# Performance work log

Measured on AMD Instinct MI355X. Metric: run time of the kernel, lower is better.

Reference implementation:

```python
import jax, jax.numpy as jnp
import numpy as np

D = 1024      # model dim
H = 16        # num heads
HD = D // H   # head dim = 64
B, N, M = 4, 4096, 256
EPS = 1e-12   # torch F.normalize eps


def setup_inputs() -> dict:
    key = jax.random.key(0)
    ks = jax.random.split(key, 11)
    s = 0.02  # weight init scale
    W = lambda k: jax.random.normal(k, (D, D), jnp.float32) * s
    return {
        "x": jax.random.normal(ks[0], (B, N, D), jnp.float32),
        "c": jax.random.normal(ks[1], (B, M, D), jnp.float32),
        "Wq_x": W(ks[2]), "Wk_x": W(ks[3]), "Wv_x": W(ks[4]),
        "Wq_c": W(ks[5]), "Wk_c": W(ks[6]), "Wv_c": W(ks[7]),
        "Wo_x": W(ks[8]), "Wo_c": W(ks[9]),
        "norm_const": 0.5 * jnp.ones((1, H, 1, 1), jnp.float32),
    }


def _heads(t):
    # (B, S, D) -> (B, H, S, HD)
    b, s, _ = t.shape
    return t.reshape(b, s, H, HD).transpose(0, 2, 1, 3)


def _l2norm(t):
    n = jnp.linalg.norm(t, axis=-1, keepdims=True)
    return t / jnp.maximum(n, EPS)


def reference(x, c, Wq_x, Wk_x, Wv_x, Wq_c, Wk_c, Wv_c, Wo_x, Wo_c, norm_const):
    b, n, d = x.shape
    m = c.shape[1]
    # fused QKV projections for each stream (Linear, no bias: y = t @ W^T)
    qx = _l2norm(_heads(x @ Wq_x.T))   # (B,H,N,HD), cosine-normalized
    kx = _l2norm(_heads(x @ Wk_x.T))
    vx = _heads(x @ Wv_x.T)
    qc = _l2norm(_heads(c @ Wq_c.T))   # (B,H,M,HD)
    kc = _l2norm(_heads(c @ Wk_c.T))
    vc = _heads(c @ Wv_c.T)
    # concat streams along the sequence axis
    q = jnp.concatenate([qx, qc], axis=2)   # (B,H,N+M,HD)
    k = jnp.concatenate([kx, kc], axis=2)
    v = jnp.concatenate([vx, vc], axis=2)
    n_tot = n + m
    # cosine (linear) attention, non-causal: values scaled by N^sigmoid(norm_const)
    v = v / (jnp.float32(n_tot) ** jax.nn.sigmoid(norm_const))
    kv = jnp.einsum("bhnd,bhne->bhde", k, v)         # (B,H,HD,HD)
    attn = jnp.einsum("bhnd,bhde->bhne", q, kv)      # (B,H,N+M,HD)
    # split streams, merge heads, output projections
    attn_x = attn[:, :, :n].transpose(0, 2, 1, 3).reshape(b, n, H * HD)
    attn_c = attn[:, :, n:].transpose(0, 2, 1, 3).reshape(b, m, H * HD)
    out_x = attn_x @ Wo_x.T
    out_c = attn_c @ Wo_c.T
    return out_x, out_c
```

## Files before the change

kernel.cpp:

```cpp
#include <hip/hip_runtime.h>
#include <cstdint>

typedef unsigned int u32;
typedef unsigned short u16;
typedef float fx4 __attribute__((ext_vector_type(4)));
typedef __bf16 bfx8 __attribute__((ext_vector_type(8)));

__device__ __forceinline__ u16 f2bf(float f) {
  u32 u = __builtin_bit_cast(u32, f);
  u32 r = (u + 0x7fffu + ((u >> 16) & 1u)) >> 16;
  return (u16)r;
}
__device__ __forceinline__ float bf2f(u16 v) {
  return __builtin_bit_cast(float, (u32)v << 16);
}
__device__ __forceinline__ void async_copy16(const void* g, void* l) {
  auto gp = reinterpret_cast<__attribute__((address_space(1))) void*>((uintptr_t)g);
  auto lp = reinterpret_cast<__attribute__((address_space(3))) void*>((uintptr_t)l);
  __builtin_amdgcn_global_load_lds(gp, lp, 16, 0, 0);
}

__global__ __launch_bounds__(256) void cvt_all(
    const float* __restrict__ x, const float* __restrict__ c,
    const float* __restrict__ w0, const float* __restrict__ w1,
    const float* __restrict__ w2, const float* __restrict__ w3,
    const float* __restrict__ w4, const float* __restrict__ w5,
    const float* __restrict__ w6, const float* __restrict__ w7,
    u16* __restrict__ xb, u16* __restrict__ cb, u16* __restrict__ wb) {
  const int i = blockIdx.x * 256 + threadIdx.x;
  const float* src;
  u16* dst;
  size_t off;
  if (i < 4194304) {
    src = x; dst = xb; off = (size_t)i;
  } else if (i < 4456448) {
    src = c; dst = cb; off = (size_t)(i - 4194304);
  } else {
    const int r = i - 4456448;
    const int wsel = r >> 18;
    off = (size_t)(r & 262143);
    switch (wsel) {
      case 0: src = w0; break; case 1: src = w1; break;
      case 2: src = w2; break; case 3: src = w3; break;
      case 4: src = w4; break; case 5: src = w5; break;
      case 6: src = w6; break; default: src = w7; break;
    }
    dst = wb + (size_t)wsel * 1048576;
  }
  const fx4 v = *(const fx4*)(src + off * 4);
  uint2 o;
  o.x = (u32)f2bf(v[0]) | ((u32)f2bf(v[1]) << 16);
  o.y = (u32)f2bf(v[2]) | ((u32)f2bf(v[3]) << 16);
  *(uint2*)(dst + off * 4) = o;
}

__device__ __forceinline__ void gemm256_core(
    const u16* __restrict__ A, const u16* __restrict__ Bw,
    long rowBase, long colBase, u16* lds, fx4 (&acc)[8][4]) {
  const int t = threadIdx.x;
  const int lane = t & 63;
  const int lr = lane & 15;
  const int quad = lane >> 4;
  const int w = t >> 6;
  const int wr = w >> 2;
  const int wc = w & 3;

  const int fA0 = t * 8;
  int dA[2];
  const u16* gA[2];
  const u16* gB[2];
#pragma unroll
  for (int r = 0; r < 2; ++r) {
    const int f = fA0 + r * 4096;
    const int row = f >> 5;
    const int gst = (f >> 3) & 3;
    const int scol = ((gst ^ (row & 3)) << 3);
    dA[r] = f;
    gA[r] = A + (size_t)(rowBase + row) * 1024 + scol;
    gB[r] = Bw + (size_t)(colBase + row) * 1024 + scol;
  }
  const int swk = (quad ^ (lr & 3)) << 3;
  const int abase = (wr * 128 + lr) * 32 + swk;
  const int bbase = 8192 + (wc * 64 + lr) * 32 + swk;

#pragma unroll
  for (int pt = 0; pt < 3; ++pt) {
    u16* slot = lds + pt * 16384;
#pragma unroll
    for (int r = 0; r < 2; ++r) {
      async_copy16(gA[r] + pt * 32, slot + dA[r]);
      async_copy16(gB[r] + pt * 32, slot + 8192 + dA[r]);
    }
  }
  asm volatile("s_waitcnt vmcnt(8)" ::: "memory");
  __builtin_amdgcn_s_barrier();
  __builtin_amdgcn_sched_barrier(0);

  for (int tt = 0; tt < 32; ++tt) {
    u16* slot = lds + (tt & 3) * 16384;
    bfx8 bfr[4], af[4];
#pragma unroll
    for (int i = 0; i < 4; ++i) bfr[i] = *(const bfx8*)(slot + bbase + i * 512);
#pragma unroll
    for (int i = 0; i < 4; ++i) af[i] = *(const bfx8*)(slot + abase + i * 512);
    if (tt < 29) {
      u16* nslot = lds + ((tt + 3) & 3) * 16384;
      const int ko = (tt + 3) * 32;
#pragma unroll
      for (int r = 0; r < 2; ++r) {
        async_copy16(gA[r] + ko, nslot + dA[r]);
        async_copy16(gB[r] + ko, nslot + 8192 + dA[r]);
      }
    }
    __builtin_amdgcn_s_setprio(1);
#pragma unroll
    for (int mi = 0; mi < 4; ++mi)
#pragma unroll
      for (int ni = 0; ni < 4; ++ni)
        acc[mi][ni] =
            __builtin_amdgcn_mfma_f32_16x16x32_bf16(af[mi], bfr[ni], acc[mi][ni], 0, 0, 0);
    __builtin_amdgcn_s_setprio(0);
#pragma unroll
    for (int i = 0; i < 4; ++i)
      af[i] = *(const bfx8*)(slot + abase + 2048 + i * 512);
    __builtin_amdgcn_s_setprio(1);
#pragma unroll
    for (int mi = 0; mi < 4; ++mi)
#pragma unroll
      for (int ni = 0; ni < 4; ++ni)
        acc[4 + mi][ni] =
            __builtin_amdgcn_mfma_f32_16x16x32_bf16(af[mi], bfr[ni], acc[4 + mi][ni], 0, 0, 0);
    __builtin_amdgcn_s_setprio(0);
    __builtin_amdgcn_sched_barrier(0);
    if (tt < 29) {
      asm volatile("s_waitcnt vmcnt(8) lgkmcnt(0)" ::: "memory");
      __builtin_amdgcn_s_barrier();
    } else if (tt == 29) {
      asm volatile("s_waitcnt vmcnt(4) lgkmcnt(0)" ::: "memory");
      __builtin_amdgcn_s_barrier();
    } else if (tt == 30) {
      asm volatile("s_waitcnt vmcnt(0) lgkmcnt(0)" ::: "memory");
      __builtin_amdgcn_s_barrier();
    }
    __builtin_amdgcn_sched_barrier(0);
  }
}

__global__ __launch_bounds__(512, 2) void proj_fused(
    const u16* __restrict__ Xb, const u16* __restrict__ Cb, const u16* __restrict__ Wb,
    u16* __restrict__ Qx, u16* __restrict__ Qc,
    u16* __restrict__ Kt, u16* __restrict__ Vt,
    const float* __restrict__ nc) {
  extern __shared__ __align__(16) u16 lds[];
  const bool isC = blockIdx.y >= 64;
  const u16* A = isC ? Cb : Xb;
  const u16* Bw = Wb + (isC ? 3145728 : 0);
  const long rowBase = (long)(isC ? blockIdx.y - 64 : blockIdx.y) * 256;
  const long colBase = (long)blockIdx.x * 256;

  fx4 acc[8][4] = {};
  gemm256_core(A, Bw, rowBase, colBase, lds, acc);

  const int t = threadIdx.x;
  const int lane = t & 63;
  const int lr = lane & 15;
  const int quad = lane >> 4;
  const int w = t >> 6;
  const int wr = w >> 2;
  const int wc = w & 3;
  const long wRowBase = rowBase + wr * 128;

  const long col0 = colBase + wc * 64;
  const int col64 = (int)(col0 >> 6);
  const int sel = col64 >> 4;
  const int h = col64 & 15;
  const int lcolBase = (int)(col0 & 1023);

  if (sel == 0) {
    u16* dst = isC ? Qc : Qx;
#pragma unroll
    for (int mi = 0; mi < 8; ++mi) {
      float ss[4] = {0.f, 0.f, 0.f, 0.f};
#pragma unroll
      for (int ni = 0; ni < 4; ++ni)
#pragma unroll
        for (int r = 0; r < 4; ++r) ss[r] += acc[mi][ni][r] * acc[mi][ni][r];
#pragma unroll
      for (int off = 1; off < 16; off <<= 1)
#pragma unroll
        for (int r = 0; r < 4; ++r) ss[r] += __shfl_xor(ss[r], off, 64);
      float sc[4];
#pragma unroll
      for (int r = 0; r < 4; ++r) sc[r] = 1.f / fmaxf(sqrtf(ss[r]), 1e-12f);
#pragma unroll
      for (int ni = 0; ni < 4; ++ni) {
        const long col = lcolBase + ni * 16 + lr;
#pragma unroll
        for (int r = 0; r < 4; ++r) {
          const long row = wRowBase + mi * 16 + quad * 4 + r;
          dst[row * 1024 + col] = f2bf(acc[mi][ni][r] * sc[r]);
        }
      }
    }
  } else {
    __syncthreads();
    u16* LT = lds + w * 8192;
    u16* T = (sel == 1) ? Kt : Vt;
    int b, nglob0;
    if (!isC) { b = (int)(wRowBase >> 12); nglob0 = (int)(wRowBase & 4095); }
    else      { b = (int)(wRowBase >> 8);  nglob0 = 4096 + (int)(wRowBase & 255); }
    u16* Tw = T + (size_t)(b * 16 + h) * 64 * 4352;
    const float vs = __expf(-8.3783908f / (1.f + __expf(-nc[h])));

#pragma unroll
    for (int mi = 0; mi < 8; ++mi) {
      float sc[4];
      if (sel == 1) {
        float ss[4] = {0.f, 0.f, 0.f, 0.f};
#pragma unroll
        for (int ni = 0; ni < 4; ++ni)
#pragma unroll
          for (int r = 0; r < 4; ++r) ss[r] += acc[mi][ni][r] * acc[mi][ni][r];
#pragma unroll
        for (int off = 1; off < 16; off <<= 1)
#pragma unroll
          for (int r = 0; r < 4; ++r) ss[r] += __shfl_xor(ss[r], off, 64);
#pragma unroll
        for (int r = 0; r < 4; ++r) sc[r] = 1.f / fmaxf(sqrtf(ss[r]), 1e-12f);
      } else {
#pragma unroll
        for (int r = 0; r < 4; ++r) sc[r] = vs;
      }
      const int g = mi * 2 + (quad >> 1);
      const int sub = (quad & 1) * 4;
#pragma unroll
      for (int ni = 0; ni < 4; ++ni) {
        const int d = ni * 16 + lr;
        uint2 o;
        o.x = (u32)f2bf(acc[mi][ni][0] * sc[0]) | ((u32)f2bf(acc[mi][ni][1] * sc[1]) << 16);
        o.y = (u32)f2bf(acc[mi][ni][2] * sc[2]) | ((u32)f2bf(acc[mi][ni][3] * sc[3]) << 16);
        *(uint2*)&LT[d * 128 + ((g ^ (d & 15)) << 3) + sub] = o;
      }
    }
    __syncthreads();
    const int d = lane;
    u16* drow = Tw + (size_t)d * 4352 + nglob0;
#pragma unroll
    for (int j = 0; j < 16; ++j) {
      const uint4 qv = *(const uint4*)&LT[d * 128 + ((j ^ (d & 15)) << 3)];
      *(uint4*)&drow[j * 8] = qv;
    }
  }
}

__global__ __launch_bounds__(256) void kv_mfma(
    const u16* __restrict__ Kt, const u16* __restrict__ Vt, float* __restrict__ kvb) {
  __shared__ __align__(16) u16 TT[4][2][4096];
  const int bh = blockIdx.x;
  const int t = threadIdx.x;
  const int w = t >> 6;
  const int lane = t & 63;
  const int lr = lane & 15;
  const int quad = lane >> 4;
  const u16* Ksrc = Kt + (size_t)bh * 64 * 4352;
  const u16* Vsrc = Vt + (size_t)bh * 64 * 4352;
  const int row8 = lane >> 3;
  const int gst = lane & 7;
  fx4 acc[4][4] = {};

  for (int s = 0; s < 17; ++s) {
    const int kbase = w * 1088 + s * 64;
#pragma unroll
    for (int i = 0; i < 8; ++i) {
      const int row = i * 8 + row8;
      const int col = ((gst ^ (row & 7)) << 3);
      const size_t go = (size_t)row * 4352 + kbase + col;
      async_copy16(Ksrc + go, &TT[w][0][i * 512 + lane * 8]);
      async_copy16(Vsrc + go, &TT[w][1][i * 512 + lane * 8]);
    }
    __syncthreads();
#pragma unroll
    for (int ks = 0; ks < 2; ++ks) {
      bfx8 af[4], bfr[4];
      const int g = ((ks * 4 + quad) ^ (lr & 7)) << 3;
#pragma unroll
      for (int i = 0; i < 4; ++i) af[i] = *(const bfx8*)&TT[w][0][(i * 16 + lr) * 64 + g];
#pragma unroll
      for (int i = 0; i < 4; ++i) bfr[i] = *(const bfx8*)&TT[w][1][(i * 16 + lr) * 64 + g];
#pragma unroll
      for (int mi = 0; mi < 4; ++mi)
#pragma unroll
        for (int ni = 0; ni < 4; ++ni)
          acc[mi][ni] =
              __builtin_amdgcn_mfma_f32_16x16x32_bf16(af[mi], bfr[ni], acc[mi][ni], 0, 0, 0);
    }
    __syncthreads();
  }
  float* red = (float*)&TT[0][0][0];
  float* my = red + w * 4096;
#pragma unroll
  for (int mi = 0; mi < 4; ++mi)
#pragma unroll
    for (int ni = 0; ni < 4; ++ni) {
      const int e = ni * 16 + lr;
      const int dg = mi * 4 + quad;
      *(fx4*)&my[e * 64 + ((dg ^ (e & 15)) << 2)] = acc[mi][ni];
    }
  __syncthreads();
  float* outp = kvb + (size_t)bh * 4096;
#pragma unroll
  for (int j = 0; j < 4; ++j) {
    const int L = t * 16 + j * 4;
    const int e = L >> 6;
    const int dg = (L >> 2) & 15;
    const int addr = e * 64 + ((dg ^ (e & 15)) << 2);
    fx4 sv = *(const fx4*)&red[addr];
    sv += *(const fx4*)&red[4096 + addr];
    sv += *(const fx4*)&red[8192 + addr];
    sv += *(const fx4*)&red[12288 + addr];
    *(fx4*)&outp[L] = sv;
  }
}

__global__ __launch_bounds__(256) void weff_build(
    const u16* __restrict__ WoX, const u16* __restrict__ WoC,
    const float* __restrict__ kvb, u16* __restrict__ WeffX, u16* __restrict__ WeffC) {
  const int ot = blockIdx.x;
  const int bh = blockIdx.y;
  const int b = bh >> 4, h = bh & 15;
  const u16* Wo = blockIdx.z ? WoC : WoX;
  u16* outp = (blockIdx.z ? WeffC : WeffX) + (size_t)b * 1048576;

  __shared__ __align__(16) float kvT[64 * 64];
  __shared__ __align__(16) float WoT[64 * 64];
  const int t = threadIdx.x;
#pragma unroll
  for (int j = 0; j < 4; ++j) {
    const int idx = (t + 256 * j) * 4;
    *(fx4*)&kvT[idx] = *(const fx4*)&kvb[(size_t)bh * 4096 + idx];
  }
#pragma unroll
  for (int j = 0; j < 2; ++j) {
    const int u = t + 256 * j;
    const int row = u >> 3;
    const int e0 = (u & 7) * 8;
    const uint4 q = *(const uint4*)&Wo[(size_t)(ot * 64 + row) * 1024 + h * 64 + e0];
    WoT[(e0 + 0) * 64 + row] = bf2f((u16)(q.x & 0xffff));
    WoT[(e0 + 1) * 64 + row] = bf2f((u16)(q.x >> 16));
    WoT[(e0 + 2) * 64 + row] = bf2f((u16)(q.y & 0xffff));
    WoT[(e0 + 3) * 64 + row] = bf2f((u16)(q.y >> 16));
    WoT[(e0 + 4) * 64 + row] = bf2f((u16)(q.z & 0xffff));
    WoT[(e0 + 5) * 64 + row] = bf2f((u16)(q.z >> 16));
    WoT[(e0 + 6) * 64 + row] = bf2f((u16)(q.w & 0xffff));
    WoT[(e0 + 7) * 64 + row] = bf2f((u16)(q.w >> 16));
  }
  __syncthreads();
  const int ob = (t >> 4) * 4;
  const int db = (t & 15) * 4;
  float acc[4][4] = {};
#pragma unroll 4
  for (int e = 0; e < 64; ++e) {
    const fx4 wv = *(const fx4*)&WoT[e * 64 + ob];
    const fx4 kvv = *(const fx4*)&kvT[e * 64 + db];
#pragma unroll
    for (int i = 0; i < 4; ++i)
#pragma unroll
      for (int j = 0; j < 4; ++j)
        acc[i][j] += wv[i] * kvv[j];
  }
#pragma unroll
  for (int i = 0; i < 4; ++i)
#pragma unroll
    for (int j = 0; j < 4; ++j)
      outp[(size_t)(ot * 64 + ob + i) * 1024 + h * 64 + db + j] = f2bf(acc[i][j]);
}

__global__ __launch_bounds__(512, 2) void out_fused(
    const u16* __restrict__ Qx, const u16* __restrict__ Qc,
    const u16* __restrict__ Wex, const u16* __restrict__ Wec,
    float* __restrict__ out) {
  extern __shared__ __align__(16) u16 lds[];
  const int yt = blockIdx.y;
  const int b = yt / 17;
  const int l = yt - b * 17;
  const bool isC = (l == 16);
  const u16* A;
  const u16* Bw;
  float* C;
  long rowBase;
  if (!isC) {
    A = Qx + (size_t)b * 4194304;
    Bw = Wex + (size_t)b * 1048576;
    C = out + (size_t)b * 4194304;
    rowBase = (long)l * 256;
  } else {
    A = Qc + (size_t)b * 262144;
    Bw = Wec + (size_t)b * 1048576;
    C = out + 16777216 + (size_t)b * 262144;
    rowBase = 0;
  }
  const long colBase = (long)blockIdx.x * 256;

  fx4 acc[8][4] = {};
  gemm256_core(A, Bw, rowBase, colBase, lds, acc);

  const int t = threadIdx.x;
  const int lane = t & 63;
  const int lr = lane & 15;
  const int quad = lane >> 4;
  const int w = t >> 6;
  const int wr = w >> 2;
  const int wc = w & 3;
#pragma unroll
  for (int mi = 0; mi < 8; ++mi)
#pragma unroll
    for (int ni = 0; ni < 4; ++ni) {
      const long col = colBase + wc * 64 + ni * 16 + lr;
#pragma unroll
      for (int r = 0; r < 4; ++r) {
        const long row = rowBase + wr * 128 + mi * 16 + quad * 4 + r;
        C[row * 1024 + col] = acc[mi][ni][r];
      }
    }
}

extern "C" void kernel_launch(void* const* d_in, const int* in_sizes, int n_in,
                              void* d_out, int out_size, void* d_ws, size_t ws_size,
                              hipStream_t stream) {
  (void)in_sizes; (void)n_in; (void)out_size; (void)ws_size;
  const float* x = (const float*)d_in[0];
  const float* c = (const float*)d_in[1];
  const float* nc = (const float*)d_in[10];
  float* out = (float*)d_out;
  char* ws = (char*)d_ws;

  static bool attr_done = false;
  if (!attr_done) {
    hipFuncSetAttribute((const void*)proj_fused,
                        hipFuncAttributeMaxDynamicSharedMemorySize, 131072);
    hipFuncSetAttribute((const void*)out_fused,
                        hipFuncAttributeMaxDynamicSharedMemorySize, 131072);
    attr_done = true;
  }

  u16* Xb = (u16*)(ws + 0);
  u16* Cb = (u16*)(ws + 33554432);
  u16* Wb = (u16*)(ws + 35651584);
  u16* Qx = (u16*)(ws + 52428800);
  u16* Qc = (u16*)(ws + 85983232);
  u16* Kt = (u16*)(ws + 88080384);
  u16* Vt = (u16*)(ws + 123731968);
  float* kvb = (float*)(ws + 159383552);
  u16* Weffx = (u16*)(ws + 160432128);
  u16* Weffc = (u16*)(ws + 168820736);

  cvt_all<<<25600, 256, 0, stream>>>(
      x, c, (const float*)d_in[2], (const float*)d_in[3], (const float*)d_in[4],
      (const float*)d_in[5], (const float*)d_in[6], (const float*)d_in[7],
      (const float*)d_in[8], (const float*)d_in[9], Xb, Cb, Wb);

  proj_fused<<<dim3(12, 68), 512, 131072, stream>>>(Xb, Cb, Wb, Qx, Qc, Kt, Vt, nc);
  kv_mfma<<<64, 256, 0, stream>>>(Kt, Vt, kvb);
  weff_build<<<dim3(16, 64, 2), 256, 0, stream>>>(Wb + 6 * 1048576, Wb + 7 * 1048576,
                                                  kvb, Weffx, Weffc);
  out_fused<<<dim3(4, 68), 512, 131072, stream>>>(Qx, Qc, Weffx, Weffc, out);
}
```

Before: 419.3 us.

## Restructure GEMM mainloop into 8-phase ping-pong schedule with new LDS swizzle

Rewrites the 256x256 bf16 GEMM core so that each iteration covers two 64-wide K blocks split into eight phases. Each phase interleaves LDS reads, async global-to-LDS copies of half an operand tile, and one half of the MFMA work, with a barrier between every phase. The LDS layout also changes: two rows are packed per 64-element line, with an XOR swizzle meant to reduce bank conflicts. The goal is finer overlap of global loads with MFMA and fewer LDS stalls, at the cost of more barriers and more complex wait-count bookkeeping, which risks errors.

```diff
diff --git a/kernel.cpp b/kernel.cpp
--- a/kernel.cpp
+++ b/kernel.cpp
@@ -54,8 +54,35 @@
   *(uint2*)(dst + off * 4) = o;
 }
 
+#define GC_DSB(BUF, KS)                                                        \
+  _Pragma("unroll") for (int i_ = 0; i_ < 4; ++i_) bfr[i_] =                   \
+      *(const bfx8*)(lds + (BUF) + 16384 + (KS) * 8192 + wc * 2048 + i_ * 512 + aLane);
+#define GC_DSA(BUF, KS, H)                                                     \
+  _Pragma("unroll") for (int i_ = 0; i_ < 4; ++i_) af[i_] =                    \
+      *(const bfx8*)(lds + (BUF) + (KS) * 8192 + wr * 4096 + (H) * 2048 + i_ * 512 + aLane);
+#define GC_STA(REG, KCOL)                                                      \
+  async_copy16(Aop + aOff0 + (KCOL), lds + (REG) + dst0);                      \
+  async_copy16(Aop + aOff1 + (KCOL), lds + (REG) + dst1);
+#define GC_STB(REG, KCOL)                                                      \
+  async_copy16(Bop + bOff0 + (KCOL), lds + (REG) + dst0);                      \
+  async_copy16(Bop + bOff1 + (KCOL), lds + (REG) + dst1);
+#define GC_MFMA(H)                                                             \
+  __builtin_amdgcn_s_setprio(1);                                               \
+  _Pragma("unroll") for (int mi_ = 0; mi_ < 4; ++mi_)                          \
+  _Pragma("unroll") for (int ni_ = 0; ni_ < 4; ++ni_)                          \
+      acc[(H) * 4 + mi_][ni_] = __builtin_amdgcn_mfma_f32_16x16x32_bf16(       \
+          af[mi_], bfr[ni_], acc[(H) * 4 + mi_][ni_], 0, 0, 0);                \
+  __builtin_amdgcn_s_setprio(0);
+#define GC_MID()                                                               \
+  __builtin_amdgcn_s_barrier();                                                \
+  asm volatile("s_waitcnt lgkmcnt(0)" ::: "memory");                           \
+  __builtin_amdgcn_sched_barrier(0);
+#define GC_END()                                                               \
+  __builtin_amdgcn_s_barrier();                                                \
+  __builtin_amdgcn_sched_barrier(0);
+
 __device__ __forceinline__ void gemm256_core(
-    const u16* __restrict__ A, const u16* __restrict__ Bw,
+    const u16* __restrict__ Aop, const u16* __restrict__ Bop,
     long rowBase, long colBase, u16* lds, fx4 (&acc)[8][4]) {
   const int t = threadIdx.x;
   const int lane = t & 63;
@@ -64,85 +91,84 @@
   const int w = t >> 6;
   const int wr = w >> 2;
   const int wc = w & 3;
-
-  const int fA0 = t * 8;
-  int dA[2];
-  const u16* gA[2];
-  const u16* gB[2];
-#pragma unroll
-  for (int r = 0; r < 2; ++r) {
-    const int f = fA0 + r * 4096;
-    const int row = f >> 5;
-    const int gst = (f >> 3) & 3;
-    const int scol = ((gst ^ (row & 3)) << 3);
-    dA[r] = f;
-    gA[r] = A + (size_t)(rowBase + row) * 1024 + scol;
-    gB[r] = Bw + (size_t)(colBase + row) * 1024 + scol;
-  }
-  const int swk = (quad ^ (lr & 3)) << 3;
-  const int abase = (wr * 128 + lr) * 32 + swk;
-  const int bbase = 8192 + (wc * 64 + lr) * 32 + swk;
-
-#pragma unroll
-  for (int pt = 0; pt < 3; ++pt) {
-    u16* slot = lds + pt * 16384;
-#pragma unroll
-    for (int r = 0; r < 2; ++r) {
-      async_copy16(gA[r] + pt * 32, slot + dA[r]);
-      async_copy16(gB[r] + pt * 32, slot + 8192 + dA[r]);
-    }
-  }
+  const int phys = (((lr & 1) << 2) | quad) ^ ((lr >> 1) & 7);
+  const int aLane = ((lr >> 1) << 6) + (phys << 3);
+
+  int aOff0, aOff1, bOff0, bOff1, dst0, dst1;
+  {
+    const int c0 = t;
+    const int R0 = c0 >> 3;
+    const int lg0 = (c0 & 7) ^ (R0 & 7);
+    const int m0_ = 2 * R0 + (lg0 >> 2);
+    const int g0 = lg0 & 3;
+    aOff0 = (int)(rowBase + m0_) * 1024 + g0 * 8;
+    bOff0 = (int)(colBase + m0_) * 1024 + g0 * 8;
+    dst0 = c0 * 8;
+    const int c1 = t + 512;
+    const int R1 = c1 >> 3;
+    const int lg1 = (c1 & 7) ^ (R1 & 7);
+    const int m1_ = 2 * R1 + (lg1 >> 2);
+    const int g1 = lg1 & 3;
+    aOff1 = (int)(rowBase + m1_) * 1024 + g1 * 8;
+    bOff1 = (int)(colBase + m1_) * 1024 + g1 * 8;
+    dst1 = c1 * 8;
+  }
+
+  GC_STA(0, 0) GC_STB(16384, 0) GC_STA(8192, 32) GC_STB(24576, 32)
+  GC_STA(32768, 64) GC_STB(49152, 64)
   asm volatile("s_waitcnt vmcnt(8)" ::: "memory");
   __builtin_amdgcn_s_barrier();
   __builtin_amdgcn_sched_barrier(0);
 
-  for (int tt = 0; tt < 32; ++tt) {
-    u16* slot = lds + (tt & 3) * 16384;
-    bfx8 bfr[4], af[4];
-#pragma unroll
-    for (int i = 0; i < 4; ++i) bfr[i] = *(const bfx8*)(slot + bbase + i * 512);
-#pragma unroll
-    for (int i = 0; i < 4; ++i) af[i] = *(const bfx8*)(slot + abase + i * 512);
-    if (tt < 29) {
-      u16* nslot = lds + ((tt + 3) & 3) * 16384;
-      const int ko = (tt + 3) * 32;
-#pragma unroll
-      for (int r = 0; r < 2; ++r) {
-        async_copy16(gA[r] + ko, nslot + dA[r]);
-        async_copy16(gB[r] + ko, nslot + 8192 + dA[r]);
-      }
-    }
-    __builtin_amdgcn_s_setprio(1);
-#pragma unroll
-    for (int mi = 0; mi < 4; ++mi)
-#pragma unroll
-      for (int ni = 0; ni < 4; ++ni)
-        acc[mi][ni] =
-            __builtin_amdgcn_mfma_f32_16x16x32_bf16(af[mi], bfr[ni], acc[mi][ni], 0, 0, 0);
-    __builtin_amdgcn_s_setprio(0);
-#pragma unroll
-    for (int i = 0; i < 4; ++i)
-      af[i] = *(const bfx8*)(slot + abase + 2048 + i * 512);
-    __builtin_amdgcn_s_setprio(1);
-#pragma unroll
-    for (int mi = 0; mi < 4; ++mi)
-#pragma unroll
-      for (int ni = 0; ni < 4; ++ni)
-        acc[4 + mi][ni] =
-            __builtin_amdgcn_mfma_f32_16x16x32_bf16(af[mi], bfr[ni], acc[4 + mi][ni], 0, 0, 0);
-    __builtin_amdgcn_s_setprio(0);
-    __builtin_amdgcn_sched_barrier(0);
-    if (tt < 29) {
-      asm volatile("s_waitcnt vmcnt(8) lgkmcnt(0)" ::: "memory");
-      __builtin_amdgcn_s_barrier();
-    } else if (tt == 29) {
-      asm volatile("s_waitcnt vmcnt(4) lgkmcnt(0)" ::: "memory");
-      __builtin_amdgcn_s_barrier();
-    } else if (tt == 30) {
-      asm volatile("s_waitcnt vmcnt(0) lgkmcnt(0)" ::: "memory");
-      __builtin_amdgcn_s_barrier();
-    }
-    __builtin_amdgcn_sched_barrier(0);
+  bfx8 bfr[4];
+  for (int it = 0; it < 8; ++it) {
+    const bool lastI = (it == 7);
+    const int k1 = (2 * it + 1) * 64 + 32;
+    const int k2 = (2 * it + 2) * 64;
+    const int k3 = k2 + 32;
+    const int k4 = (2 * it + 3) * 64;
+    { bfx8 af[4];
+      GC_DSB(0, 0) GC_DSA(0, 0, 0)
+      GC_STA(40960, k1)
+      GC_MID() GC_MFMA(0) GC_END() }
+    { bfx8 af[4];
+      GC_DSA(0, 0, 1)
+      GC_STB(57344, k1)
+      GC_MID() GC_MFMA(1)
+      asm volatile("s_waitcnt vmcnt(8)" ::: "memory");
+      GC_END() }
+    { bfx8 af[4];
+      GC_DSB(0, 1) GC_DSA(0, 1, 0)
+      if (!lastI) { GC_STA(0, k2) }
+      GC_MID() GC_MFMA(0) GC_END() }
+    { bfx8 af[4];
+      GC_DSA(0, 1, 1)
+      if (!lastI) { GC_STB(16384, k2) }
+      GC_MID() GC_MFMA(1)
+      if (lastI) { asm volatile("s_waitcnt vmcnt(4)" ::: "memory"); }
+      else       { asm volatile("s_waitcnt vmcnt(8)" ::: "memory"); }
+      GC_END() }
+    { bfx8 af[4];
+      GC_DSB(32768, 0) GC_DSA(32768, 0, 0)
+      if (!lastI) { GC_STA(8192, k3) }
+      GC_MID() GC_MFMA(0) GC_END() }
+    { bfx8 af[4];
+      GC_DSA(32768, 0, 1)
+      if (!lastI) { GC_STB(24576, k3) }
+      GC_MID() GC_MFMA(1)
+      if (lastI) { asm volatile("s_waitcnt vmcnt(0)" ::: "memory"); }
+      else       { asm volatile("s_waitcnt vmcnt(8)" ::: "memory"); }
+      GC_END() }
+    { bfx8 af[4];
+      GC_DSB(32768, 1) GC_DSA(32768, 1, 0)
+      if (!lastI) { GC_STA(32768, k4) }
+      GC_MID() GC_MFMA(0) GC_END() }
+    { bfx8 af[4];
+      GC_DSA(32768, 1, 1)
+      if (!lastI) { GC_STB(49152, k4) }
+      GC_MID() GC_MFMA(1)
+      if (!lastI) { asm volatile("s_waitcnt vmcnt(8)" ::: "memory"); }
+      GC_END() }
   }
 }
 
```

Result: faster. 408.7 us (-2.5%).
